# Performance work log

Hardware: AMD Instinct MI355X
Metric: run time of the kernel (lower is better)

## Reference

```python
import jax, jax.numpy as jnp
import numpy as np
from jax import lax

NUM_WORD, NUM_TAG, EMB, HID, SEQ = 50000, 50, 500, 200, 4096
START, END = 48, 49
NEG = -10000.0


def setup_inputs() -> dict:
    key = jax.random.key(0)
    ks = jax.random.split(key, 16)
    s = 0.1  # weight scale for numerical sanity
    trans = jax.random.normal(ks[13], (NUM_TAG, NUM_TAG), jnp.float32)
    trans = trans.at[START, :].set(NEG).at[:, END].set(NEG)
    return {
        'sentence_ids': jax.random.randint(ks[0], (1, SEQ), 0, NUM_WORD),
        'tags_ids': jax.random.randint(ks[1], (SEQ,), 0, START),
        'embedding': jax.random.normal(ks[2], (NUM_WORD, EMB), jnp.float32),
        'w_ih_f': s * jax.random.normal(ks[3], (4 * HID, EMB), jnp.float32),
        'w_hh_f': s * jax.random.normal(ks[4], (4 * HID, HID), jnp.float32),
        'b_ih_f': s * jax.random.normal(ks[5], (4 * HID,), jnp.float32),
        'b_hh_f': s * jax.random.normal(ks[6], (4 * HID,), jnp.float32),
        'w_ih_b': s * jax.random.normal(ks[7], (4 * HID, EMB), jnp.float32),
        'w_hh_b': s * jax.random.normal(ks[8], (4 * HID, HID), jnp.float32),
        'b_ih_b': s * jax.random.normal(ks[9], (4 * HID,), jnp.float32),
        'b_hh_b': s * jax.random.normal(ks[10], (4 * HID,), jnp.float32),
        'linear_w': s * jax.random.normal(ks[11], (NUM_TAG, 2 * HID), jnp.float32),
        'linear_b': s * jax.random.normal(ks[12], (NUM_TAG,), jnp.float32),
        'transitions': trans,
        'h0': jax.random.normal(ks[14], (2, HID), jnp.float32),
        'c0': jax.random.normal(ks[15], (2, HID), jnp.float32),
    }


def _lstm_dir(x_proj, w_hh, h0, c0):
    # x_proj: [S, 4H] precomputed input projection (+ both biases)
    def step(carry, xp):
        h, c = carry
        g = xp + h @ w_hh.T  # [4H], torch gate order i,f,g,o
        i, f, gg, o = jnp.split(g, 4)
        c = jax.nn.sigmoid(f) * c + jax.nn.sigmoid(i) * jnp.tanh(gg)
        h = jax.nn.sigmoid(o) * jnp.tanh(c)
        return (h, c), h
    _, hs = lax.scan(step, (h0, c0), x_proj)
    return hs  # [S, H]


def _get_feats(sentence_ids, embedding, w_ih_f, w_hh_f, b_ih_f, b_hh_f,
               w_ih_b, w_hh_b, b_ih_b, b_hh_b, linear_w, linear_b, h0, c0):
    x = embedding[sentence_ids[0]]  # [S, EMB]
    xf = x @ w_ih_f.T + (b_ih_f + b_hh_f)  # one big GEMM, fold hh-bias in
    xb = x[::-1] @ w_ih_b.T + (b_ih_b + b_hh_b)
    hf = _lstm_dir(xf, w_hh_f, h0[0], c0[0])          # [S, H]
    hb = _lstm_dir(xb, w_hh_b, h0[1], c0[1])[::-1]    # [S, H]
    h = jnp.concatenate([hf, hb], axis=-1)            # [S, 2H]
    return h @ linear_w.T + linear_b                   # [S, NUM_TAG]


def _crf_forward(feats, transitions):
    alpha = jnp.full((NUM_TAG,), NEG, feats.dtype).at[START].set(0.0)
    def step(alpha, feat):
        smat = alpha[:, None] + transitions + feat[None, :]  # [T, T]
        return jax.nn.logsumexp(smat, axis=0), None
    alpha, _ = lax.scan(step, alpha, feats)
    return jax.nn.logsumexp(alpha + transitions[:, END])


def _gold_score(feats, tags_ids, transitions):
    tags = jnp.concatenate([jnp.array([START], tags_ids.dtype), tags_ids])
    trans_sc = transitions[tags[:-1], tags[1:]].sum()
    emit_sc = feats[jnp.arange(feats.shape[0]), tags[1:]].sum()
    return trans_sc + emit_sc + transitions[tags[-1], END]


def _viterbi(feats, transitions):
    alpha = jnp.full((NUM_TAG,), NEG, feats.dtype).at[START].set(0.0)
    def step(alpha, feat):
        smat = alpha[:, None] + feat[None, :] + transitions  # [T, T]
        return smat.max(axis=0), smat.argmax(axis=0)
    alpha, bp = lax.scan(step, alpha, feats)  # bp: [S, T]
    fin = alpha + transitions[:, END]
    best = jnp.argmax(fin)
    def bt(tag, bp_t):
        prev = bp_t[tag]
        return prev, prev
    _, prevs = lax.scan(bt, best, bp[1:][::-1])  # skip first frame, as torch
    path = jnp.concatenate([prevs[::-1], best[None]])  # [S]
    return fin[best], path


def reference(sentence_ids, tags_ids, embedding, w_ih_f, w_hh_f, b_ih_f, b_hh_f,
              w_ih_b, w_hh_b, b_ih_b, b_hh_b, linear_w, linear_b, transitions,
              h0, c0):
    feats = _get_feats(sentence_ids, embedding, w_ih_f, w_hh_f, b_ih_f, b_hh_f,
                       w_ih_b, w_hh_b, b_ih_b, b_hh_b, linear_w, linear_b, h0, c0)
    fwd_score = _crf_forward(feats, transitions)
    gold = _gold_score(feats, tags_ids, transitions)
    _, tag_seq = _viterbi(feats, transitions)
    loss = jnp.reshape(fwd_score - gold, (1,))
    return (tag_seq, loss)
```

## Files before the change

kernel.cpp:

```cpp
#include <hip/hip_runtime.h>

typedef unsigned int u32;
typedef unsigned char u8;

#define TSTART 48
#define TEND   49
#define NEGV  -10000.0f

#define O_XG     0ull
#define O_WIHF   4194304ull
#define O_WIHB   5013504ull
#define O_WHHF   5832704ull
#define O_WHHB   6193152ull
#define O_BSF    6553600ull
#define O_BSB    6556800ull
#define O_LWP    6560000ull
#define O_XF     6600000ull
#define O_XB     19707200ull
#define O_HT     32814400ull
#define O_FEATS  36091200ull
#define O_BP     36910400ull
#define O_FMAP   37115200ull
#define O_BTAG   37118400ull
#define O_SCAL   37118656ull

typedef _Float16 h2 __attribute__((ext_vector_type(2)));

__device__ __forceinline__ float fdot2(u32 a, u32 b, float c) {
#if defined(__HIP_DEVICE_COMPILE__) && __has_builtin(__builtin_amdgcn_fdot2)
    return __builtin_amdgcn_fdot2(__builtin_bit_cast(h2, a), __builtin_bit_cast(h2, b), c, false);
#else
    float d;
    asm("v_dot2_f32_f16 %0, %1, %2, %3" : "=v"(d) : "v"(a), "v"(b), "v"(c));
    return d;
#endif
}

__device__ __forceinline__ u32 pack2(float a, float b) {
    u32 lo = __builtin_bit_cast(unsigned short, (_Float16)a);
    u32 hi = __builtin_bit_cast(unsigned short, (_Float16)b);
    return lo | (hi << 16);
}

__device__ __forceinline__ float sigf(float x) { return 1.f / (1.f + __expf(-x)); }
__device__ __forceinline__ float tanhf_(float x) { return 2.f / (1.f + __expf(-2.f * x)) - 1.f; }

#define PA_END   90112
#define PB_END   180224
#define PC_END   385024
#define PD_END   589824
#define PE_END   1638400
#define PF_END   1648400
#define PG_END   1649200
#define PH_END   1650000

__global__ __launch_bounds__(256) void k_prep(
    const int* __restrict__ ids, const float* __restrict__ emb,
    const float* __restrict__ wihf, const float* __restrict__ wihb,
    const float* __restrict__ whhf, const float* __restrict__ whhb,
    const float* __restrict__ bihf, const float* __restrict__ bhhf,
    const float* __restrict__ bihb, const float* __restrict__ bhhb,
    const float* __restrict__ lw,
    u32* __restrict__ xg, u32* __restrict__ wif16, u32* __restrict__ wib16,
    u32* __restrict__ whf16, u32* __restrict__ whb16, u32* __restrict__ lwp,
    float* __restrict__ bsf, float* __restrict__ bsb)
{
    int idx = blockIdx.x * 256 + threadIdx.x;
    if (idx < PB_END) {
        int dirb = (idx >= PA_END);
        int i = idx - (dirb ? PA_END : 0);
        const float* whh = dirb ? whhb : whhf;
        u32* dst = dirb ? whb16 : whf16;
        int chunk = i / 176, off = i % 176;
        int rgrp = chunk >> 2, ks = chunk & 3;
        u32 v = 0;
        if (off < 175) {
            int m, kd;
            if (off < 168) { int q = off >> 2, e = off & 3; kd = ks * 25 + (q / 7) * 4 + e; m = q % 7; }
            else           { m = off - 168; kd = ks * 25 + 24; }
            int row = rgrp * 7 + m;
            if (row < 800) v = pack2(whh[row * 200 + 2 * kd], whh[row * 200 + 2 * kd + 1]);
        }
        dst[i] = v;
    } else if (idx < PD_END) {
        int dirb = (idx >= PC_END);
        int i = idx - (dirb ? PC_END : PB_END);
        const float* wih = dirb ? wihb : wihf;
        u32* dst = dirb ? wib16 : wif16;
        int r = i >> 8, d = i & 255;
        dst[i] = (d < 250) ? pack2(wih[r * 500 + 2 * d], wih[r * 500 + 2 * d + 1]) : 0u;
    } else if (idx < PE_END) {
        int i = idx - PD_END; int s = i >> 8, d = i & 255;
        long id = ids[s];
        xg[i] = (d < 250) ? pack2(emb[id * 500 + 2 * d], emb[id * 500 + 2 * d + 1]) : 0u;
    } else if (idx < PF_END) {
        int i = idx - PE_END; int tag = i / 200, u = i % 200;
        lwp[i] = pack2(lw[tag * 400 + 2 * u], lw[tag * 400 + 2 * u + 1]);
    } else if (idx < PG_END) {
        int j = idx - PF_END; bsf[j] = bihf[j] + bhhf[j];
    } else if (idx < PH_END) {
        int j = idx - PG_END; bsb[j] = bihb[j] + bhhb[j];
    }
}

__global__ __launch_bounds__(256, 2) void k_gemm(
    const u32* __restrict__ xg, const u32* __restrict__ wf, const u32* __restrict__ wb,
    const float* __restrict__ bsf, const float* __restrict__ bsb,
    float* __restrict__ xf, float* __restrict__ xb)
{
    int z = blockIdx.z;
    const u32* W = z ? wb : wf;
    const float* bs = z ? bsb : bsf;
    float* out = z ? xb : xf;
    int m0 = blockIdx.x * 256, n0 = blockIdx.y * 128;
    int t = threadIdx.x;

    __shared__ u32 As[16][256];
    __shared__ u32 Bs[16][128];

    float acc[16][8];
#pragma unroll
    for (int m = 0; m < 16; m++)
#pragma unroll
        for (int n = 0; n < 8; n++) acc[m][n] = 0.f;

    int arow = m0 + t; if (z) arow = 4095 - arow;
    const u32* aptr = xg + (size_t)arow * 256;
    int bj = n0 + (t >> 1);
    int ko = (t & 1) * 8;
    const u32* bptr = W + (size_t)bj * 256 + ko;

    int ry = t >> 4, cx = t & 15;

    for (int kc = 0; kc < 16; ++kc) {
        int kd = kc * 16;
        uint4 a0 = *(const uint4*)(aptr + kd);
        uint4 a1 = *(const uint4*)(aptr + kd + 4);
        uint4 a2 = *(const uint4*)(aptr + kd + 8);
        uint4 a3 = *(const uint4*)(aptr + kd + 12);
        uint4 bv0 = {0,0,0,0}, bv1 = {0,0,0,0};
        if (bj < 800) { bv0 = *(const uint4*)(bptr + kd); bv1 = *(const uint4*)(bptr + kd + 4); }
        __syncthreads();
        u32 ad[16] = {a0.x,a0.y,a0.z,a0.w, a1.x,a1.y,a1.z,a1.w,
                      a2.x,a2.y,a2.z,a2.w, a3.x,a3.y,a3.z,a3.w};
#pragma unroll
        for (int i = 0; i < 16; i++) As[i][t] = ad[i];
        u32 bd[8] = {bv0.x,bv0.y,bv0.z,bv0.w, bv1.x,bv1.y,bv1.z,bv1.w};
#pragma unroll
        for (int i = 0; i < 8; i++) Bs[ko + i][t >> 1] = bd[i];
        __syncthreads();
#pragma unroll
        for (int d = 0; d < 16; ++d) {
            const u32* ar = &As[d][ry * 16];
            uint4 x0 = *(const uint4*)(ar);
            uint4 x1 = *(const uint4*)(ar + 4);
            uint4 x2 = *(const uint4*)(ar + 8);
            uint4 x3 = *(const uint4*)(ar + 12);
            const u32* br = &Bs[d][cx * 8];
            uint4 y0 = *(const uint4*)(br);
            uint4 y1 = *(const uint4*)(br + 4);
            u32 am[16] = {x0.x,x0.y,x0.z,x0.w, x1.x,x1.y,x1.z,x1.w,
                          x2.x,x2.y,x2.z,x2.w, x3.x,x3.y,x3.z,x3.w};
            u32 bn[8] = {y0.x,y0.y,y0.z,y0.w, y1.x,y1.y,y1.z,y1.w};
#pragma unroll
            for (int m = 0; m < 16; m++)
#pragma unroll
                for (int n = 0; n < 8; n++)
                    acc[m][n] = fdot2(am[m], bn[n], acc[m][n]);
        }
    }
    int col = n0 + cx * 8;
    if (col < 800) {
        float4 bi0 = *(const float4*)(bs + col);
        float4 bi1 = *(const float4*)(bs + col + 4);
#pragma unroll
        for (int m = 0; m < 16; m++) {
            size_t ro = (size_t)(m0 + ry * 16 + m) * 800 + col;
            float4 o0 = {acc[m][0]+bi0.x, acc[m][1]+bi0.y, acc[m][2]+bi0.z, acc[m][3]+bi0.w};
            float4 o1 = {acc[m][4]+bi1.x, acc[m][5]+bi1.y, acc[m][6]+bi1.z, acc[m][7]+bi1.w};
            *(float4*)(out + ro) = o0;
            *(float4*)(out + ro + 4) = o1;
        }
    }
}


#define LOAD_WROW(c) \
    uint4 W##c##0 = p[(c)*7+0], W##c##1 = p[(c)*7+1], W##c##2 = p[(c)*7+2], \
          W##c##3 = p[(c)*7+3], W##c##4 = p[(c)*7+4], W##c##5 = p[(c)*7+5], \
          W##c##6 = p[(c)*7+6];

#define DOTQ(Wv, A) \
    A = fdot2(Wv.x, hb.x, A); A = fdot2(Wv.y, hb.y, A); \
    A = fdot2(Wv.z, hb.z, A); A = fdot2(Wv.w, hb.w, A);

#define DOT_BLOCK(c) { \
    uint4 hb = *(const uint4*)(hbase + (c)*4); \
    DOTQ(W##c##0, acc0) DOTQ(W##c##1, acc1) DOTQ(W##c##2, acc2) DOTQ(W##c##3, acc3) \
    DOTQ(W##c##4, acc4) DOTQ(W##c##5, acc5) DOTQ(W##c##6, acc6) }

#define REDUCE(A) A += __shfl_xor(A, 1); A += __shfl_xor(A, 2);

__global__ __launch_bounds__(512)
__attribute__((amdgpu_waves_per_eu(2, 2)))
void k_lstm(
    const u32* __restrict__ whf, const u32* __restrict__ whb,
    const float* __restrict__ xf, const float* __restrict__ xb,
    const float* __restrict__ h0, const float* __restrict__ c0,
    u32* __restrict__ hallT)
{
    int dir = blockIdx.x, t = threadIdx.x;
    const u32* Wh = dir ? whb : whf;
    const float* xp = dir ? xb : xf;
    int ks = t & 3, rgrp = t >> 2, r0 = rgrp * 7;

    const uint4* p = (const uint4*)(Wh + (size_t)t * 176);
    LOAD_WROW(0) LOAD_WROW(1) LOAD_WROW(2) LOAD_WROW(3) LOAD_WROW(4) LOAD_WROW(5)
    const u32* p1 = Wh + (size_t)t * 176 + 168;
    u32 U0 = p1[0], U1 = p1[1], U2 = p1[2], U3 = p1[3], U4 = p1[4], U5 = p1[5], U6 = p1[6];

    __shared__ __align__(16) u32 hsh[112];
    __shared__ float gsh[800];
    __shared__ u32 hstage[800];

    if (t < 112) hsh[t] = 0u;
    __syncthreads();

    float cst = 0.f;
    int haddr = 0;
    if (t < 200) {
        cst = c0[dir * 200 + t];
        int u = t >> 1;
        haddr = (u / 25) * 28 + (u % 25);
        if (!(t & 1)) hsh[haddr] = pack2(h0[dir * 200 + t], h0[dir * 200 + t + 1]);
    }
    __syncthreads();

    const u32* hbase = hsh + ks * 28;

    for (int s = 0; s < 4096; ++s) {
        float xr0 = 0.f, xr1 = 0.f, xr2 = 0.f, xr3 = 0.f;
        if (t < 200) {
            size_t xo = (size_t)s * 800 + t;
            xr0 = xp[xo]; xr1 = xp[xo + 200]; xr2 = xp[xo + 400]; xr3 = xp[xo + 600];
        }
        if ((s & 7) == 0 && s && t < 100) {
            int s0 = s - 8;
            u32 a0 = hstage[t],       a1 = hstage[100 + t], a2 = hstage[200 + t], a3 = hstage[300 + t];
            u32 a4 = hstage[400 + t], a5 = hstage[500 + t], a6 = hstage[600 + t], a7 = hstage[700 + t];
            uint4* dst;
            uint4 v0, v1;
            if (dir == 0) {
                dst = (uint4*)(hallT + (size_t)t * 4096 + s0);
                v0 = (uint4){a0, a1, a2, a3}; v1 = (uint4){a4, a5, a6, a7};
            } else {
                dst = (uint4*)(hallT + (size_t)(100 + t) * 4096 + (4088 - s0));
                v0 = (uint4){a7, a6, a5, a4}; v1 = (uint4){a3, a2, a1, a0};
            }
            dst[0] = v0; dst[1] = v1;
        }

        float acc0 = 0.f, acc1 = 0.f, acc2 = 0.f, acc3 = 0.f, acc4 = 0.f, acc5 = 0.f, acc6 = 0.f;
        DOT_BLOCK(0) DOT_BLOCK(1) DOT_BLOCK(2) DOT_BLOCK(3) DOT_BLOCK(4) DOT_BLOCK(5)
        {
            u32 hb1 = hbase[24];
            acc0 = fdot2(U0, hb1, acc0); acc1 = fdot2(U1, hb1, acc1);
            acc2 = fdot2(U2, hb1, acc2); acc3 = fdot2(U3, hb1, acc3);
            acc4 = fdot2(U4, hb1, acc4); acc5 = fdot2(U5, hb1, acc5);
            acc6 = fdot2(U6, hb1, acc6);
        }
        REDUCE(acc0) REDUCE(acc1) REDUCE(acc2) REDUCE(acc3) REDUCE(acc4) REDUCE(acc5) REDUCE(acc6)
        if (ks == 0 && r0 < 800) {
            gsh[r0] = acc0;
            if (r0 + 1 < 800) gsh[r0 + 1] = acc1;
            if (r0 + 2 < 800) gsh[r0 + 2] = acc2;
            if (r0 + 3 < 800) gsh[r0 + 3] = acc3;
            if (r0 + 4 < 800) gsh[r0 + 4] = acc4;
            if (r0 + 5 < 800) gsh[r0 + 5] = acc5;
            if (r0 + 6 < 800) gsh[r0 + 6] = acc6;
        }
        __syncthreads();

        if (t < 200) {
            float gi = gsh[t] + xr0, gf = gsh[200 + t] + xr1;
            float gg = gsh[400 + t] + xr2, go = gsh[600 + t] + xr3;
            float is = sigf(gi), fs = sigf(gf), gt = tanhf_(gg), os = sigf(go);
            cst = fs * cst + is * gt;
            float hv = os * tanhf_(cst);
            float hq = __shfl_xor(hv, 1);
            if (!(t & 1)) {
                u32 pv = pack2(hv, hq);
                hsh[haddr] = pv;
                hstage[(s & 7) * 100 + (t >> 1)] = pv;
            }
        }
        __syncthreads();
    }
    if (t < 100) {
        u32 a0 = hstage[t],       a1 = hstage[100 + t], a2 = hstage[200 + t], a3 = hstage[300 + t];
        u32 a4 = hstage[400 + t], a5 = hstage[500 + t], a6 = hstage[600 + t], a7 = hstage[700 + t];
        uint4* dst;
        uint4 v0, v1;
        if (dir == 0) {
            dst = (uint4*)(hallT + (size_t)t * 4096 + 4088);
            v0 = (uint4){a0, a1, a2, a3}; v1 = (uint4){a4, a5, a6, a7};
        } else {
            dst = (uint4*)(hallT + (size_t)(100 + t) * 4096);
            v0 = (uint4){a7, a6, a5, a4}; v1 = (uint4){a3, a2, a1, a0};
        }
        dst[0] = v0; dst[1] = v1;
    }
}

__global__ __launch_bounds__(64) void k_linear(
    const u32* __restrict__ hallT, const u32* __restrict__ lwp,
    const float* __restrict__ lb, float* __restrict__ feats)
{
    int s = blockIdx.x, t = threadIdx.x;
    __shared__ __align__(16) u32 hc[200];
#pragma unroll
    for (int k = 0; k < 4; k++) {
        int u = t + 64 * k;
        if (u < 200) hc[u] = hallT[(size_t)u * 4096 + s];
    }
    __syncthreads();
    if (t < 50) {
        const uint4* wp = (const uint4*)(lwp + t * 200);
        const uint4* hp = (const uint4*)hc;
        float acc = lb[t];
#pragma unroll 10
        for (int c = 0; c < 50; c++) {
            uint4 wv = wp[c]; uint4 hv = hp[c];
            acc = fdot2(wv.x, hv.x, acc); acc = fdot2(wv.y, hv.y, acc);
            acc = fdot2(wv.z, hv.z, acc); acc = fdot2(wv.w, hv.w, acc);
        }
        feats[(size_t)s * 50 + t] = acc;
    }
}

__global__ __launch_bounds__(512) void k_crf(
    const float* __restrict__ feats, const float* __restrict__ trans,
    const int* __restrict__ tags, u8* __restrict__ bp, float* __restrict__ scal)
{
    __shared__ float tl[2500];
    __shared__ float al[2][64];
    __shared__ float red[512];
    int t = threadIdx.x;
    for (int i = t; i < 2500; i += 512) tl[i] = trans[i];
    __syncthreads();

    int role = blockIdx.x;
    if (role == 2) {
        float loc = 0.f;
        for (int i = t; i < 4096; i += 512) {
            int prev = i ? tags[i - 1] : TSTART;
            int cur = tags[i];
            loc += tl[prev * 50 + cur] + feats[(size_t)i * 50 + cur];
        }
        red[t] = loc; __syncthreads();
        for (int w = 256; w > 0; w >>= 1) { if (t < w) red[t] += red[t + w]; __syncthreads(); }
        if (t == 0) scal[1] = red[0] + tl[tags[4095] * 50 + TEND];
        return;
    }

    int j = t >> 3, q = t & 7;
    bool jv = j < 50;
    float Tc[7];
#pragma unroll
    for (int r = 0; r < 7; r++) {
        int i = q + 8 * r;
        Tc[r] = (jv && i < 50) ? tl[i * 50 + j] : 0.f;
    }
    if (t < 64) al[0][t] = (t == TSTART) ? 0.f : NEGV;
    __syncthreads();

    int cur = 0;
    float fcur = 0.f;
    if (q == 0 && jv) fcur = feats[j];

    if (role == 0) {
        for (int s = 0; s < 4096; ++s) {
            float fnext = 0.f;
            if (s + 1 < 4096 && q == 0 && jv) fnext = feats[(size_t)(s + 1) * 50 + j];
            float v[7]; float m = -3.0e38f;
#pragma unroll
            for (int r = 0; r < 7; r++) {
                int i = q + 8 * r;
                float vv = (i < 50) ? al[cur][i] + Tc[r] : -3.0e38f;
                v[r] = vv; m = fmaxf(m, vv);
            }
            m = fmaxf(m, __shfl_xor(m, 1));
            m = fmaxf(m, __shfl_xor(m, 2));
            m = fmaxf(m, __shfl_xor(m, 4));
            float sum = 0.f;
#pragma unroll
            for (int r = 0; r < 7; r++) {
                int i = q + 8 * r;
                if (i < 50) sum += __expf(v[r] - m);
            }
            sum += __shfl_xor(sum, 1);
            sum += __shfl_xor(sum, 2);
            sum += __shfl_xor(sum, 4);
            if (q == 0 && jv) al[cur ^ 1][j] = fcur + m + __logf(sum);
            fcur = fnext; cur ^= 1;
            __syncthreads();
        }
        if (t == 0) {
            float m = -3.0e38f;
            for (int i = 0; i < 50; i++) m = fmaxf(m, al[cur][i] + tl[i * 50 + TEND]);
            float sm = 0.f;
            for (int i = 0; i < 50; i++) sm += __expf(al[cur][i] + tl[i * 50 + TEND] - m);
            scal[0] = m + __logf(sm);
        }
    } else {
        for (int s = 0; s < 4096; ++s) {
            float fnext = 0.f;
            if (s + 1 < 4096 && q == 0 && jv) fnext = feats[(size_t)(s + 1) * 50 + j];
            float m = -3.0e38f; int mi = 63;
#pragma unroll
            for (int r = 0; r < 7; r++) {
                int i = q + 8 * r;
                float vv = (i < 50) ? al[cur][i] + Tc[r] : -3.0e38f;
                if (vv > m) { m = vv; mi = i; }
            }
#pragma unroll
            for (int k = 1; k < 8; k <<= 1) {
                float om = __shfl_xor(m, k); int oi = __shfl_xor(mi, k);
                if (om > m || (om == m && oi < mi)) { m = om; mi = oi; }
            }
            if (q == 0 && jv) {
                al[cur ^ 1][j] = m + fcur;
                bp[(size_t)s * 50 + j] = (u8)mi;
            }
            fcur = fnext; cur ^= 1;
            __syncthreads();
        }
        if (t == 0) {
            float best = -3.0e38f; int bi = 0;
            for (int i = 0; i < 50; i++) {
                float f = al[cur][i] + tl[i * 50 + TEND];
                if (f > best) { best = f; bi = i; }
            }
            ((int*)scal)[2] = bi;
        }
    }
}

__global__ __launch_bounds__(64) void k_maps(const u8* __restrict__ bp, u8* __restrict__ fmap)
{
    __shared__ __align__(4) u8 bpl[3200];
    int c = blockIdx.x, t = threadIdx.x;
    const u32* src = (const u32*)(bp + (size_t)c * 3200);
    u32* dst = (u32*)bpl;
    for (int i = t; i < 800; i += 64) dst[i] = src[i];
    __syncthreads();
    if (t < 50) {
        int y = t;
        for (int k = 63; k >= 0; --k) y = bpl[k * 50 + y];
        fmap[c * 50 + t] = (u8)y;
    }
}

__global__ __launch_bounds__(64) void k_chase(const u8* __restrict__ fmap, const float* __restrict__ scal,
                                              u8* __restrict__ btag, float* __restrict__ dout)
{
    __shared__ __align__(4) u8 fl[3200];
    int t = threadIdx.x;
    for (int i = t; i < 800; i += 64) ((u32*)fl)[i] = ((const u32*)fmap)[i];
    __syncthreads();
    if (t == 0) {
        int b = ((const int*)scal)[2];
        btag[63] = (u8)b;
        for (int c = 63; c >= 1; --c) { b = fl[c * 50 + b]; btag[c - 1] = (u8)b; }
        dout[4096] = scal[0] - scal[1];
    }
}

__global__ __launch_bounds__(64) void k_replay(const u8* __restrict__ bp, const u8* __restrict__ btag,
                                               float* __restrict__ dout)
{
    __shared__ __align__(4) u8 bpl[3200];
    int c = blockIdx.x, t = threadIdx.x;
    for (int i = t; i < 800; i += 64) ((u32*)bpl)[i] = ((const u32*)(bp + (size_t)c * 3200))[i];
    __syncthreads();
    if (t == 0) {
        int y = btag[c];
        dout[c * 64 + 63] = (float)y;
        for (int k = 62; k >= 0; --k) {
            y = bpl[(k + 1) * 50 + y];
            dout[c * 64 + k] = (float)y;
        }
    }
}

extern "C" void kernel_launch(void* const* d_in, const int* in_sizes, int n_in,
                              void* d_out, int out_size, void* d_ws, size_t ws_size,
                              hipStream_t stream)
{
    const int*   ids   = (const int*)d_in[0];
    const int*   tags  = (const int*)d_in[1];
    const float* emb   = (const float*)d_in[2];
    const float* wihf  = (const float*)d_in[3];
    const float* whhf  = (const float*)d_in[4];
    const float* bihf  = (const float*)d_in[5];
    const float* bhhf  = (const float*)d_in[6];
    const float* wihb  = (const float*)d_in[7];
    const float* whhb  = (const float*)d_in[8];
    const float* bihb  = (const float*)d_in[9];
    const float* bhhb  = (const float*)d_in[10];
    const float* lw    = (const float*)d_in[11];
    const float* lb    = (const float*)d_in[12];
    const float* trans = (const float*)d_in[13];
    const float* h0    = (const float*)d_in[14];
    const float* c0    = (const float*)d_in[15];
    float* dout = (float*)d_out;

    char* w = (char*)d_ws;
    u32*   xg    = (u32*)(w + O_XG);
    u32*   wif16 = (u32*)(w + O_WIHF);
    u32*   wib16 = (u32*)(w + O_WIHB);
    u32*   whf16 = (u32*)(w + O_WHHF);
    u32*   whb16 = (u32*)(w + O_WHHB);
    float* bsf   = (float*)(w + O_BSF);
    float* bsb   = (float*)(w + O_BSB);
    u32*   lwp   = (u32*)(w + O_LWP);
    float* xf    = (float*)(w + O_XF);
    float* xb    = (float*)(w + O_XB);
    u32*   hallT = (u32*)(w + O_HT);
    float* feats = (float*)(w + O_FEATS);
    u8*    bp    = (u8*)(w + O_BP);
    u8*    fmap  = (u8*)(w + O_FMAP);
    u8*    btag  = (u8*)(w + O_BTAG);
    float* scal  = (float*)(w + O_SCAL);

    k_prep<<<6446, 256, 0, stream>>>(ids, emb, wihf, wihb, whhf, whhb,
                                     bihf, bhhf, bihb, bhhb, lw,
                                     xg, wif16, wib16, whf16, whb16, lwp, bsf, bsb);
    k_gemm<<<dim3(16, 7, 2), 256, 0, stream>>>(xg, wif16, wib16, bsf, bsb, xf, xb);
    k_lstm<<<2, 512, 0, stream>>>(whf16, whb16, xf, xb, h0, c0, hallT);
    k_linear<<<4096, 64, 0, stream>>>(hallT, lwp, lb, feats);
    k_crf<<<3, 512, 0, stream>>>(feats, trans, tags, bp, scal);
    k_maps<<<64, 64, 0, stream>>>(bp, fmap);
    k_chase<<<1, 64, 0, stream>>>(fmap, scal, btag, dout);
    k_replay<<<64, 64, 0, stream>>>(bp, btag, dout);
}
```

Baseline: 7.561 ms.

## Split LSTM recurrent dot products across 8 K-slices with 1024-thread blocks

The recurrent LSTM kernel now runs 1024 threads per direction instead of 512. Each row group of 7 gate rows splits its K dimension across 8 threads rather than 4, and the fp16 weight repacking, h shared-memory layout and reduction shuffles change to match. This halves the serial dot-product chain and the register-resident weights per thread, aiming to shorten each of the 4096 sequential steps. In exchange it adds one more shuffle stage per accumulator and puts more waves into each block barrier, which could offset the gain.

```diff
diff --git a/kernel.cpp b/kernel.cpp
--- a/kernel.cpp
+++ b/kernel.cpp
@@ -11,18 +11,18 @@
 #define O_WIHF   4194304ull
 #define O_WIHB   5013504ull
 #define O_WHHF   5832704ull
-#define O_WHHB   6193152ull
-#define O_BSF    6553600ull
-#define O_BSB    6556800ull
-#define O_LWP    6560000ull
-#define O_XF     6600000ull
-#define O_XB     19707200ull
-#define O_HT     32814400ull
-#define O_FEATS  36091200ull
-#define O_BP     36910400ull
-#define O_FMAP   37115200ull
-#define O_BTAG   37118400ull
-#define O_SCAL   37118656ull
+#define O_WHHB   6209536ull
+#define O_BSF    6586368ull
+#define O_BSB    6589568ull
+#define O_LWP    6592768ull
+#define O_XF     6632768ull
+#define O_XB     19739968ull
+#define O_HT     32847168ull
+#define O_FEATS  36123968ull
+#define O_BP     36943168ull
+#define O_FMAP   37147968ull
+#define O_BTAG   37151168ull
+#define O_SCAL   37151424ull
 
 typedef _Float16 h2 __attribute__((ext_vector_type(2)));
 
@@ -45,14 +45,14 @@
 __device__ __forceinline__ float sigf(float x) { return 1.f / (1.f + __expf(-x)); }
 __device__ __forceinline__ float tanhf_(float x) { return 2.f / (1.f + __expf(-2.f * x)) - 1.f; }
 
-#define PA_END   90112
-#define PB_END   180224
-#define PC_END   385024
-#define PD_END   589824
-#define PE_END   1638400
-#define PF_END   1648400
-#define PG_END   1649200
-#define PH_END   1650000
+#define PA_END   94208
+#define PB_END   188416
+#define PC_END   393216
+#define PD_END   598016
+#define PE_END   1646592
+#define PF_END   1656592
+#define PG_END   1657392
+#define PH_END   1658192
 
 __global__ __launch_bounds__(256) void k_prep(
     const int* __restrict__ ids, const float* __restrict__ emb,
@@ -71,15 +71,15 @@
         int i = idx - (dirb ? PA_END : 0);
         const float* whh = dirb ? whhb : whhf;
         u32* dst = dirb ? whb16 : whf16;
-        int chunk = i / 176, off = i % 176;
-        int rgrp = chunk >> 2, ks = chunk & 3;
+        int chunk = i / 92, off = i % 92;
+        int rgrp = chunk >> 3, ks = chunk & 7;
         u32 v = 0;
-        if (off < 175) {
+        if (off < 91) {
             int m, kd;
-            if (off < 168) { int q = off >> 2, e = off & 3; kd = ks * 25 + (q / 7) * 4 + e; m = q % 7; }
-            else           { m = off - 168; kd = ks * 25 + 24; }
+            if (off < 84) { int q = off >> 2, e = off & 3; int c4 = q / 7; m = q % 7; kd = ks * 13 + c4 * 4 + e; }
+            else          { m = off - 84; kd = ks * 13 + 12; }
             int row = rgrp * 7 + m;
-            if (row < 800) v = pack2(whh[row * 200 + 2 * kd], whh[row * 200 + 2 * kd + 1]);
+            if (row < 800 && kd < 100) v = pack2(whh[row * 200 + 2 * kd], whh[row * 200 + 2 * kd + 1]);
         }
         dst[i] = v;
     } else if (idx < PD_END) {
@@ -199,10 +199,10 @@
     DOTQ(W##c##0, acc0) DOTQ(W##c##1, acc1) DOTQ(W##c##2, acc2) DOTQ(W##c##3, acc3) \
     DOTQ(W##c##4, acc4) DOTQ(W##c##5, acc5) DOTQ(W##c##6, acc6) }
 
-#define REDUCE(A) A += __shfl_xor(A, 1); A += __shfl_xor(A, 2);
-
-__global__ __launch_bounds__(512)
-__attribute__((amdgpu_waves_per_eu(2, 2)))
+#define REDUCE(A) A += __shfl_xor(A, 1); A += __shfl_xor(A, 2); A += __shfl_xor(A, 4);
+
+__global__ __launch_bounds__(1024, 4)
+__attribute__((amdgpu_waves_per_eu(4, 4)))
 void k_lstm(
     const u32* __restrict__ whf, const u32* __restrict__ whb,
     const float* __restrict__ xf, const float* __restrict__ xb,
@@ -212,18 +212,18 @@
     int dir = blockIdx.x, t = threadIdx.x;
     const u32* Wh = dir ? whb : whf;
     const float* xp = dir ? xb : xf;
-    int ks = t & 3, rgrp = t >> 2, r0 = rgrp * 7;
-
-    const uint4* p = (const uint4*)(Wh + (size_t)t * 176);
-    LOAD_WROW(0) LOAD_WROW(1) LOAD_WROW(2) LOAD_WROW(3) LOAD_WROW(4) LOAD_WROW(5)
-    const u32* p1 = Wh + (size_t)t * 176 + 168;
+    int ks = t & 7, rgrp = t >> 3, r0 = rgrp * 7;
+
+    const uint4* p = (const uint4*)(Wh + (size_t)t * 92);
+    LOAD_WROW(0) LOAD_WROW(1) LOAD_WROW(2)
+    const u32* p1 = Wh + (size_t)t * 92 + 84;
     u32 U0 = p1[0], U1 = p1[1], U2 = p1[2], U3 = p1[3], U4 = p1[4], U5 = p1[5], U6 = p1[6];
 
-    __shared__ __align__(16) u32 hsh[112];
-    __shared__ float gsh[800];
+    __shared__ __align__(16) u32 hsh[160];
+    __shared__ float gsh[896];
     __shared__ u32 hstage[800];
 
-    if (t < 112) hsh[t] = 0u;
+    if (t < 160) hsh[t] = 0u;
     __syncthreads();
 
     float cst = 0.f;
@@ -231,12 +231,12 @@
     if (t < 200) {
         cst = c0[dir * 200 + t];
         int u = t >> 1;
-        haddr = (u / 25) * 28 + (u % 25);
+        haddr = (u / 13) * 20 + (u % 13);
         if (!(t & 1)) hsh[haddr] = pack2(h0[dir * 200 + t], h0[dir * 200 + t + 1]);
     }
     __syncthreads();
 
-    const u32* hbase = hsh + ks * 28;
+    const u32* hbase = hsh + ks * 20;
 
     for (int s = 0; s < 4096; ++s) {
         float xr0 = 0.f, xr1 = 0.f, xr2 = 0.f, xr3 = 0.f;
@@ -261,23 +261,19 @@
         }
 
         float acc0 = 0.f, acc1 = 0.f, acc2 = 0.f, acc3 = 0.f, acc4 = 0.f, acc5 = 0.f, acc6 = 0.f;
-        DOT_BLOCK(0) DOT_BLOCK(1) DOT_BLOCK(2) DOT_BLOCK(3) DOT_BLOCK(4) DOT_BLOCK(5)
+        DOT_BLOCK(0) DOT_BLOCK(1) DOT_BLOCK(2)
         {
-            u32 hb1 = hbase[24];
-            acc0 = fdot2(U0, hb1, acc0); acc1 = fdot2(U1, hb1, acc1);
-            acc2 = fdot2(U2, hb1, acc2); acc3 = fdot2(U3, hb1, acc3);
-            acc4 = fdot2(U4, hb1, acc4); acc5 = fdot2(U5, hb1, acc5);
-            acc6 = fdot2(U6, hb1, acc6);
+            u32 hb = hbase[12];
+            acc0 = fdot2(U0, hb, acc0); acc1 = fdot2(U1, hb, acc1);
+            acc2 = fdot2(U2, hb, acc2); acc3 = fdot2(U3, hb, acc3);
+            acc4 = fdot2(U4, hb, acc4); acc5 = fdot2(U5, hb, acc5);
+            acc6 = fdot2(U6, hb, acc6);
         }
         REDUCE(acc0) REDUCE(acc1) REDUCE(acc2) REDUCE(acc3) REDUCE(acc4) REDUCE(acc5) REDUCE(acc6)
-        if (ks == 0 && r0 < 800) {
-            gsh[r0] = acc0;
-            if (r0 + 1 < 800) gsh[r0 + 1] = acc1;
-            if (r0 + 2 < 800) gsh[r0 + 2] = acc2;
-            if (r0 + 3 < 800) gsh[r0 + 3] = acc3;
-            if (r0 + 4 < 800) gsh[r0 + 4] = acc4;
-            if (r0 + 5 < 800) gsh[r0 + 5] = acc5;
-            if (r0 + 6 < 800) gsh[r0 + 6] = acc6;
+        if (ks == 0) {
+            gsh[r0]     = acc0; gsh[r0 + 1] = acc1; gsh[r0 + 2] = acc2;
+            gsh[r0 + 3] = acc3; gsh[r0 + 4] = acc4; gsh[r0 + 5] = acc5;
+            gsh[r0 + 6] = acc6;
         }
         __syncthreads();
 
@@ -533,11 +529,11 @@
     u8*    btag  = (u8*)(w + O_BTAG);
     float* scal  = (float*)(w + O_SCAL);
 
-    k_prep<<<6446, 256, 0, stream>>>(ids, emb, wihf, wihb, whhf, whhb,
+    k_prep<<<6478, 256, 0, stream>>>(ids, emb, wihf, wihb, whhf, whhb,
                                      bihf, bhhf, bihb, bhhb, lw,
                                      xg, wif16, wib16, whf16, whb16, lwp, bsf, bsb);
     k_gemm<<<dim3(16, 7, 2), 256, 0, stream>>>(xg, wif16, wib16, bsf, bsb, xf, xb);
-    k_lstm<<<2, 512, 0, stream>>>(whf16, whb16, xf, xb, h0, c0, hallT);
+    k_lstm<<<2, 1024, 0, stream>>>(whf16, whb16, xf, xb, h0, c0, hallT);
     k_linear<<<4096, 64, 0, stream>>>(hallT, lwp, lb, feats);
     k_crf<<<3, 512, 0, stream>>>(feats, trans, tags, bp, scal);
     k_maps<<<64, 64, 0, stream>>>(bp, fmap);
```

New measurement: 10.11 ms. 33.7% more time.

## Spill part of recurrent LSTM weights into LDS to cut register pressure

Applied to the files above, without the earlier changes.

Moves roughly the first half of each thread's packed fp16 recurrent weights (19 uint4 per thread) from registers into a large shared-memory buffer, keeping the rest in registers, and interleaves LDS-sourced and register-sourced dot blocks. It also drops the waves_per_eu(2,2) attribute. The aim is to lower VGPR usage and possible spilling in the sequential recurrence loop. In exchange every timestep adds many LDS reads, and the roughly 156KB LDS buffer may exceed per-block limits or add latency on the critical serial path.

```diff
diff --git a/kernel.cpp b/kernel.cpp
--- a/kernel.cpp
+++ b/kernel.cpp
@@ -185,24 +185,15 @@
 }
 
 
-#define LOAD_WROW(c) \
-    uint4 W##c##0 = p[(c)*7+0], W##c##1 = p[(c)*7+1], W##c##2 = p[(c)*7+2], \
-          W##c##3 = p[(c)*7+3], W##c##4 = p[(c)*7+4], W##c##5 = p[(c)*7+5], \
-          W##c##6 = p[(c)*7+6];
-
 #define DOTQ(Wv, A) \
     A = fdot2(Wv.x, hb.x, A); A = fdot2(Wv.y, hb.y, A); \
     A = fdot2(Wv.z, hb.z, A); A = fdot2(Wv.w, hb.w, A);
 
-#define DOT_BLOCK(c) { \
-    uint4 hb = *(const uint4*)(hbase + (c)*4); \
-    DOTQ(W##c##0, acc0) DOTQ(W##c##1, acc1) DOTQ(W##c##2, acc2) DOTQ(W##c##3, acc3) \
-    DOTQ(W##c##4, acc4) DOTQ(W##c##5, acc5) DOTQ(W##c##6, acc6) }
+#define DOT_LDS_ROW(off, A) { uint4 w = *(const uint4*)(wl + (off)); DOTQ(w, A) }
 
 #define REDUCE(A) A += __shfl_xor(A, 1); A += __shfl_xor(A, 2);
 
 __global__ __launch_bounds__(512)
-__attribute__((amdgpu_waves_per_eu(2, 2)))
 void k_lstm(
     const u32* __restrict__ whf, const u32* __restrict__ whb,
     const float* __restrict__ xf, const float* __restrict__ xb,
@@ -214,14 +205,22 @@
     const float* xp = dir ? xb : xf;
     int ks = t & 3, rgrp = t >> 2, r0 = rgrp * 7;
 
-    const uint4* p = (const uint4*)(Wh + (size_t)t * 176);
-    LOAD_WROW(0) LOAD_WROW(1) LOAD_WROW(2) LOAD_WROW(3) LOAD_WROW(4) LOAD_WROW(5)
-    const u32* p1 = Wh + (size_t)t * 176 + 168;
-    u32 U0 = p1[0], U1 = p1[1], U2 = p1[2], U3 = p1[3], U4 = p1[4], U5 = p1[5], U6 = p1[6];
-
+    __shared__ __align__(16) u32 wlds[512 * 76];
     __shared__ __align__(16) u32 hsh[112];
     __shared__ float gsh[800];
     __shared__ u32 hstage[800];
+
+    const uint4* p = (const uint4*)(Wh + (size_t)t * 176);
+    u32* wl = wlds + t * 76;
+#pragma unroll
+    for (int i = 0; i < 19; ++i) *(uint4*)(wl + i * 4) = p[i];
+
+    uint4 R0  = p[19], R1  = p[20];
+    uint4 R2  = p[21], R3  = p[22], R4  = p[23], R5  = p[24], R6  = p[25], R7  = p[26], R8  = p[27];
+    uint4 R9  = p[28], R10 = p[29], R11 = p[30], R12 = p[31], R13 = p[32], R14 = p[33], R15 = p[34];
+    uint4 R16 = p[35], R17 = p[36], R18 = p[37], R19 = p[38], R20 = p[39], R21 = p[40], R22 = p[41];
+    const u32* p1 = Wh + (size_t)t * 176 + 168;
+    u32 U0 = p1[0], U1 = p1[1], U2 = p1[2], U3 = p1[3], U4 = p1[4], U5 = p1[5], U6 = p1[6];
 
     if (t < 112) hsh[t] = 0u;
     __syncthreads();
@@ -261,7 +260,39 @@
         }
 
         float acc0 = 0.f, acc1 = 0.f, acc2 = 0.f, acc3 = 0.f, acc4 = 0.f, acc5 = 0.f, acc6 = 0.f;
-        DOT_BLOCK(0) DOT_BLOCK(1) DOT_BLOCK(2) DOT_BLOCK(3) DOT_BLOCK(4) DOT_BLOCK(5)
+        {
+            uint4 hb = *(const uint4*)(hbase + 0);
+            DOT_LDS_ROW(0,  acc0) DOT_LDS_ROW(4,  acc1) DOT_LDS_ROW(8,  acc2)
+            DOT_LDS_ROW(12, acc3) DOT_LDS_ROW(16, acc4) DOT_LDS_ROW(20, acc5)
+            DOT_LDS_ROW(24, acc6)
+        }
+        {
+            uint4 hb = *(const uint4*)(hbase + 12);
+            DOTQ(R2, acc0) DOTQ(R3, acc1) DOTQ(R4, acc2) DOTQ(R5, acc3)
+            DOTQ(R6, acc4) DOTQ(R7, acc5) DOTQ(R8, acc6)
+        }
+        {
+            uint4 hb = *(const uint4*)(hbase + 4);
+            DOT_LDS_ROW(28, acc0) DOT_LDS_ROW(32, acc1) DOT_LDS_ROW(36, acc2)
+            DOT_LDS_ROW(40, acc3) DOT_LDS_ROW(44, acc4) DOT_LDS_ROW(48, acc5)
+            DOT_LDS_ROW(52, acc6)
+        }
+        {
+            uint4 hb = *(const uint4*)(hbase + 16);
+            DOTQ(R9,  acc0) DOTQ(R10, acc1) DOTQ(R11, acc2) DOTQ(R12, acc3)
+            DOTQ(R13, acc4) DOTQ(R14, acc5) DOTQ(R15, acc6)
+        }
+        {
+            uint4 hb = *(const uint4*)(hbase + 8);
+            DOT_LDS_ROW(56, acc0) DOT_LDS_ROW(60, acc1) DOT_LDS_ROW(64, acc2)
+            DOT_LDS_ROW(68, acc3) DOT_LDS_ROW(72, acc4)
+            DOTQ(R0, acc5) DOTQ(R1, acc6)
+        }
+        {
+            uint4 hb = *(const uint4*)(hbase + 20);
+            DOTQ(R16, acc0) DOTQ(R17, acc1) DOTQ(R18, acc2) DOTQ(R19, acc3)
+            DOTQ(R20, acc4) DOTQ(R21, acc5) DOTQ(R22, acc6)
+        }
         {
             u32 hb1 = hbase[24];
             acc0 = fdot2(U0, hb1, acc0); acc1 = fdot2(U1, hb1, acc1);
```

Measured after the change: 8.528 ms. 1.13x slower.
